# Kernel optimization log

Measured on AMD Instinct MI355X. Metric: run time of the kernel, lower is better.

The kernel has to match this reference:

```python
import jax, jax.numpy as jnp
import numpy as np

HIDDEN = 1024
CUTOFFS = [20000, 80000, 200000]
PROJECT_FACTOR = 4
NUM_TAILS = len(CUTOFFS) - 1
CUTOFF_ENDS = [0] + CUTOFFS
BATCH, SEQ = 8, 1024


def _glorot(key, shape):
    fan_in, fan_out = shape
    limit = np.sqrt(6.0 / (fan_in + fan_out)).astype(np.float32)
    return jax.random.uniform(key, shape, jnp.float32, -limit, limit)


def setup_inputs() -> dict:
    key = jax.random.key(0)
    ks = jax.random.split(key, 7)
    return {
        "x": jax.random.randint(ks[0], (BATCH, SEQ), 0, CUTOFFS[-1], dtype=jnp.int64.dtype if jax.config.jax_enable_x64 else jnp.int32),
        "head_weight_proj": _glorot(ks[1], (HIDDEN, HIDDEN)),
        "head_weight": _glorot(ks[2], (HIDDEN, CUTOFFS[0] + NUM_TAILS)),
        "tail_weight_proj_0": _glorot(ks[3], (HIDDEN, HIDDEN // PROJECT_FACTOR)),
        "tail_weight_0": _glorot(ks[4], (HIDDEN // PROJECT_FACTOR, CUTOFFS[1] - CUTOFFS[0])),
        "tail_weight_proj_1": _glorot(ks[5], (HIDDEN, HIDDEN // PROJECT_FACTOR ** 2)),
        "tail_weight_1": _glorot(ks[6], (HIDDEN // PROJECT_FACTOR ** 2, CUTOFFS[2] - CUTOFFS[1])),
    }


def reference(x, head_weight_proj, head_weight, tail_weight_proj_0,
              tail_weight_0, tail_weight_proj_1, tail_weight_1) -> jnp.ndarray:
    # Faithful to AdaptiveEmbedding.compute_embeddings:
    #   tables[i] = weight.T (head truncated to cutoffs[0] rows), projs[i] = proj.T
    #   per-cluster: gather rows of table for in-range ids, matmul with proj,
    #   scatter back into y; here expressed densely with masks (same math,
    #   fixed shapes; out-of-cluster tokens contribute exactly zero).
    tables = [head_weight.T[:CUTOFFS[0]], tail_weight_0.T, tail_weight_1.T]
    projs = [head_weight_proj.T, tail_weight_proj_0.T, tail_weight_proj_1.T]
    y = jnp.zeros(x.shape + (HIDDEN,), dtype=jnp.float32)
    for i in range(len(CUTOFF_ENDS) - 1):
        l_idx, r_idx = CUTOFF_ENDS[i], CUTOFF_ENDS[i + 1]
        mask = (x >= l_idx) & (x < r_idx)                  # [B,S]
        idx = jnp.where(mask, x - l_idx, 0)                # in-range gather ids
        emb = tables[i][idx]                               # [B,S,d_i]
        proj = jnp.einsum('bsd,dh->bsh', emb, projs[i])    # [B,S,H]
        y = y + jnp.where(mask[..., None], proj, 0.0)
    emb_scale = jnp.asarray(HIDDEN ** 0.5, y.dtype)
    return y * emb_scale
```

## Files before the change

kernel.cpp:

```cpp
#include <hip/hip_runtime.h>
#include <hip/hip_bf16.h>

#define NTOK 8192
#define HID 1024
#define C0_END 20000
#define C1_END 80000
#define S0 20002
#define S1 60000
#define S2 120000

#define CAP0 1280
#define CAP1 3072
#define CAP2 6144
#define TS0 (CAP0/32)
#define TS1 (CAP1/32)
#define TS2 (CAP2/32)

#define NBUCK 12500

#define OFF_CNT 0
#define OFF_SST 16
#define OFF_BB  32
#define OFF_LS  50048
#define OFF_LI  (OFF_LS + NTOK*3*4)
#define OFF_W0  (OFF_LI + NTOK*3*4)
#define OFF_W1  (OFF_W0 + 1024*1024*2)
#define OFF_W2  (OFF_W1 + 256*1024*2)
#define OFF_A0  (OFF_W2 + 64*1024*2)
#define OFF_A1  (OFF_A0 + CAP0*1024*2)
#define OFF_A2  (OFF_A1 + CAP1*256*2)

typedef __attribute__((ext_vector_type(8))) short bf16x8;
typedef __attribute__((ext_vector_type(8))) unsigned short ushort8;
typedef __attribute__((ext_vector_type(4))) float f32x4;

__device__ __forceinline__ unsigned short f2bf(float f) {
    union { __hip_bfloat16 b; unsigned short u; } cv;
    cv.b = __float2bfloat16(f);
    return cv.u;
}


__global__ void k_init(unsigned* __restrict__ bb, int* __restrict__ cnt) {
    int gid = blockIdx.x * 256 + threadIdx.x, stride = gridDim.x * 256;
    for (int i = gid; i < NBUCK; i += stride) bb[i] = 0u;
    if (gid < 3) cnt[gid] = 0;
}

__global__ void k_count(const int* __restrict__ x, int* __restrict__ cnt,
                        unsigned* __restrict__ bb) {
    int s = blockIdx.x * 256 + threadIdx.x;
    int lane = threadIdx.x & 63;
    int v = x[s];
    atomicAdd(&bb[v >> 4], 1u);
    int c = (v < C0_END) ? 0 : (v < C1_END ? 1 : 2);
    unsigned long long m0 = __ballot(c == 0);
    unsigned long long m1 = __ballot(c == 1);
    unsigned long long m2 = __ballot(c == 2);
    unsigned long long mymask = (c == 0) ? m0 : (c == 1) ? m1 : m2;
    int leader = __builtin_ctzll(mymask);
    if (lane == leader) atomicAdd(&cnt[c], __popcll(mymask));
}

__global__ __launch_bounds__(1024) void k_scan(unsigned* __restrict__ bb,
                                               unsigned* __restrict__ sstart) {
    __shared__ unsigned psum[16];
    int t = threadIdx.x, lane = t & 63, w = t >> 6;
    int base = t * 13;
    unsigned loc[13];
    unsigned s = 0;
#pragma unroll
    for (int i = 0; i < 13; i++) {
        int idx = base + i;
        unsigned v = (idx < NBUCK) ? bb[idx] : 0u;
        loc[i] = v; s += v;
    }
    unsigned inc = s;
    for (int d = 1; d < 64; d <<= 1) {
        unsigned o = __shfl_up(inc, d);
        if (lane >= d) inc += o;
    }
    if (lane == 63) psum[w] = inc;
    __syncthreads();
    if (w == 0) {
        unsigned ws = (lane < 16) ? psum[lane] : 0u;
        for (int d = 1; d < 16; d <<= 1) {
            unsigned o = __shfl_up(ws, d);
            if (lane >= d) ws += o;
        }
        if (lane < 16) psum[lane] = ws;
    }
    __syncthreads();
    unsigned excl = inc - s + ((w > 0) ? psum[w - 1] : 0u);
#pragma unroll
    for (int i = 0; i < 13; i++) {
        int idx = base + i;
        if (idx < NBUCK) bb[idx] = excl;
        excl += loc[i];
    }
    __syncthreads();
    if (t == 0) { sstart[0] = 0u; sstart[1] = bb[1250]; sstart[2] = bb[5000]; }
}

__global__ void k_scatter(const int* __restrict__ x, unsigned* __restrict__ bb,
                          const unsigned* __restrict__ sstart,
                          int* __restrict__ ls, int* __restrict__ li) {
    int s = blockIdx.x * 256 + threadIdx.x;
    int v = x[s];
    int c    = (v < C0_END) ? 0 : (v < C1_END ? 1 : 2);
    int base = (c == 0) ? 0 : (c == 1) ? C0_END : C1_END;
    unsigned cap = (c == 0) ? CAP0 : (c == 1) ? CAP1 : CAP2;
    unsigned pos = atomicAdd(&bb[v >> 4], 1u) - sstart[c];
    if (pos < cap) {
        ls[c * NTOK + pos] = s;
        li[c * NTOK + pos] = v - base;
    }
}

template <int KS>
__device__ __forceinline__ size_t frag_off(int m, int k8) {
    return ((size_t)(((m >> 5) * KS + (k8 >> 2)) * 2 + ((m >> 4) & 1)) << 9)
         + (size_t)(((m & 15) + (k8 & 3) * 16) * 8);
}

template <int KS, int S, int MGSH>
__device__ __forceinline__ void spread_item(int e, int mi, int ki, int n,
                                            const float* __restrict__ t,
                                            const int* __restrict__ li,
                                            unsigned short* __restrict__ A) {
    int mg  = e >> MGSH;
    int k8g = e & ((1 << MGSH) - 1);
    int m  = mg * 8 + mi;
    int k8 = k8g * 8 + ki;
    int idx = (m < n) ? li[m] : 0;
    const float* src = t + (size_t)(k8 * 8) * S + idx;
    ushort8 v = {0, 0, 0, 0, 0, 0, 0, 0};
    if (m < n) {
#pragma unroll
        for (int j = 0; j < 8; j++) v[j] = f2bf(src[(size_t)j * S]);
    }
    *(ushort8*)(A + frag_off<KS>(m, k8)) = v;
}

__global__ void k_gather(const float* __restrict__ t0, const float* __restrict__ t1,
                         const float* __restrict__ t2,
                         const float* __restrict__ hwp, const float* __restrict__ twp0,
                         const float* __restrict__ twp1,
                         const int* __restrict__ cnt, const int* __restrict__ li,
                         unsigned short* __restrict__ A0, unsigned short* __restrict__ A1,
                         unsigned short* __restrict__ A2,
                         unsigned short* __restrict__ W0, unsigned short* __restrict__ W1,
                         unsigned short* __restrict__ W2) {
    int gid = blockIdx.x * 256 + threadIdx.x, stride = gridDim.x * 256;
    for (int i = gid; i < (1024 * 1024) / 4; i += stride) {
        float4 v = ((const float4*)hwp)[i];
        ushort4 o = { f2bf(v.x), f2bf(v.y), f2bf(v.z), f2bf(v.w) };
        ((ushort4*)W0)[i] = o;
    }
    for (int i = gid; i < (1024 * 256) / 4; i += stride) {
        float4 v = ((const float4*)twp0)[i];
        ushort4 o = { f2bf(v.x), f2bf(v.y), f2bf(v.z), f2bf(v.w) };
        ((ushort4*)W1)[i] = o;
    }
    for (int i = gid; i < (1024 * 64) / 4; i += stride) {
        float4 v = ((const float4*)twp1)[i];
        ushort4 o = { f2bf(v.x), f2bf(v.y), f2bf(v.z), f2bf(v.w) };
        ((ushort4*)W2)[i] = o;
    }
    int n0 = min(cnt[0], CAP0), n1 = min(cnt[1], CAP1), n2 = min(cnt[2], CAP2);
    int r0 = ((n0 + 31) >> 5) << 5;
    int r1 = ((n1 + 31) >> 5) << 5;
    int r2 = ((n2 + 31) >> 5) << 5;
    int i0 = r0 * 2;
    int i1 = r1 / 2;
    int i2 = r2 / 8;
    int tot = i0 + i1 + i2;
    int lane = threadIdx.x & 63;
    int mi = lane >> 3, ki = lane & 7;
    int wid = blockIdx.x * (blockDim.x >> 6) + (threadIdx.x >> 6);
    int nw  = gridDim.x * (blockDim.x >> 6);
    for (int it = wid; it < tot; it += nw) {
        if (it < i0)
            spread_item<32, S0, 4>(it, mi, ki, n0, t0, li, A0);
        else if (it < i0 + i1)
            spread_item<8, S1, 2>(it - i0, mi, ki, n1, t1, li + NTOK, A1);
        else
            spread_item<2, S2, 0>(it - i0 - i1, mi, ki, n2, t2, li + 2 * NTOK, A2);
    }
}

template <int K>
__device__ __forceinline__ void gemm_body(int tile, int n, int lane, int wave, int by,
                                          const unsigned short* __restrict__ Ap,
                                          const unsigned short* __restrict__ Wb,
                                          const int* __restrict__ ls,
                                          float* __restrict__ out) {
    constexpr int KS = K / 32;
    int m0 = tile * 32;
    int lr = lane & 15, lg = lane >> 4;
    int hb = by * 256 + wave * 64;
    const unsigned short* abase = Ap + (size_t)tile * KS * 1024 + lane * 8;
    const unsigned short* bbase = Wb + (size_t)(hb + lr) * K + lg * 8;
    f32x4 acc[2][4] = {};
#pragma unroll 4
    for (int ks = 0; ks < KS; ks++) {
        bf16x8 a0 = *(const bf16x8*)(abase + ks * 1024);
        bf16x8 a1 = *(const bf16x8*)(abase + ks * 1024 + 512);
        bf16x8 b0 = *(const bf16x8*)(bbase + ks * 32);
        bf16x8 b1 = *(const bf16x8*)(bbase + ks * 32 + 16 * K);
        bf16x8 b2 = *(const bf16x8*)(bbase + ks * 32 + 32 * K);
        bf16x8 b3 = *(const bf16x8*)(bbase + ks * 32 + 48 * K);
        acc[0][0] = __builtin_amdgcn_mfma_f32_16x16x32_bf16(a0, b0, acc[0][0], 0, 0, 0);
        acc[0][1] = __builtin_amdgcn_mfma_f32_16x16x32_bf16(a0, b1, acc[0][1], 0, 0, 0);
        acc[0][2] = __builtin_amdgcn_mfma_f32_16x16x32_bf16(a0, b2, acc[0][2], 0, 0, 0);
        acc[0][3] = __builtin_amdgcn_mfma_f32_16x16x32_bf16(a0, b3, acc[0][3], 0, 0, 0);
        acc[1][0] = __builtin_amdgcn_mfma_f32_16x16x32_bf16(a1, b0, acc[1][0], 0, 0, 0);
        acc[1][1] = __builtin_amdgcn_mfma_f32_16x16x32_bf16(a1, b1, acc[1][1], 0, 0, 0);
        acc[1][2] = __builtin_amdgcn_mfma_f32_16x16x32_bf16(a1, b2, acc[1][2], 0, 0, 0);
        acc[1][3] = __builtin_amdgcn_mfma_f32_16x16x32_bf16(a1, b3, acc[1][3], 0, 0, 0);
    }
#pragma unroll
    for (int mf = 0; mf < 2; mf++)
#pragma unroll
        for (int r = 0; r < 4; r++) {
            int m = mf * 16 + lg * 4 + r;
            if (m0 + m < n) {
                int s = ls[m0 + m];
                float* orow = out + (size_t)s * HID + hb + lr;
                orow[0]  = 32.f * acc[mf][0][r];
                orow[16] = 32.f * acc[mf][1][r];
                orow[32] = 32.f * acc[mf][2][r];
                orow[48] = 32.f * acc[mf][3][r];
            }
        }
}

__global__ __launch_bounds__(256) void k_gemm(const int* __restrict__ cnt,
                                              const int* __restrict__ ls,
                                              const unsigned short* __restrict__ A0,
                                              const unsigned short* __restrict__ A1,
                                              const unsigned short* __restrict__ A2,
                                              const unsigned short* __restrict__ W0,
                                              const unsigned short* __restrict__ W1,
                                              const unsigned short* __restrict__ W2,
                                              float* __restrict__ out) {
    int bx = blockIdx.x;
    int lane = threadIdx.x & 63, wave = threadIdx.x >> 6;
    if (bx < TS0) {
        int n = min(cnt[0], CAP0); if (bx * 32 >= n) return;
        gemm_body<1024>(bx, n, lane, wave, blockIdx.y, A0, W0, ls, out);
    } else if (bx < TS0 + TS1) {
        int t = bx - TS0;
        int n = min(cnt[1], CAP1); if (t * 32 >= n) return;
        gemm_body<256>(t, n, lane, wave, blockIdx.y, A1, W1, ls + NTOK, out);
    } else {
        int t = bx - TS0 - TS1;
        int n = min(cnt[2], CAP2); if (t * 32 >= n) return;
        gemm_body<64>(t, n, lane, wave, blockIdx.y, A2, W2, ls + 2 * NTOK, out);
    }
}

extern "C" void kernel_launch(void* const* d_in, const int* in_sizes, int n_in,
                              void* d_out, int out_size, void* d_ws, size_t ws_size,
                              hipStream_t stream) {
    const int*   x    = (const int*)d_in[0];
    const float* hwp  = (const float*)d_in[1];
    const float* hw   = (const float*)d_in[2];
    const float* twp0 = (const float*)d_in[3];
    const float* tw0  = (const float*)d_in[4];
    const float* twp1 = (const float*)d_in[5];
    const float* tw1  = (const float*)d_in[6];

    char* ws = (char*)d_ws;
    int* cnt          = (int*)(ws + OFF_CNT);
    unsigned* sstart  = (unsigned*)(ws + OFF_SST);
    unsigned* bb      = (unsigned*)(ws + OFF_BB);
    int* ls           = (int*)(ws + OFF_LS);
    int* li           = (int*)(ws + OFF_LI);
    unsigned short* W0 = (unsigned short*)(ws + OFF_W0);
    unsigned short* W1 = (unsigned short*)(ws + OFF_W1);
    unsigned short* W2 = (unsigned short*)(ws + OFF_W2);
    unsigned short* A0 = (unsigned short*)(ws + OFF_A0);
    unsigned short* A1 = (unsigned short*)(ws + OFF_A1);
    unsigned short* A2 = (unsigned short*)(ws + OFF_A2);
    float* out = (float*)d_out;

    k_init<<<64, 256, 0, stream>>>(bb, cnt);
    k_count<<<NTOK / 256, 256, 0, stream>>>(x, cnt, bb);
    k_scan<<<1, 1024, 0, stream>>>(bb, sstart);
    k_scatter<<<NTOK / 256, 256, 0, stream>>>(x, bb, sstart, ls, li);
    k_gather<<<1024, 256, 0, stream>>>(hw, tw0, tw1, hwp, twp0, twp1,
                                       cnt, li, A0, A1, A2, W0, W1, W2);
    k_gemm<<<dim3(TS0 + TS1 + TS2, 4), 256, 0, stream>>>(
        cnt, ls, A0, A1, A2, W0, W1, W2, out);
}
```

Measured before the change: 78.50 us.

## Fuse bucket-sort preprocessing into one kernel using shared-memory histogram

Replaces the four preprocessing kernels (init, count, scan, scatter) with a single kernel. Block 0 does the histogram, scan and scatter entirely in shared memory, while the other 256 blocks convert the projection weights to bf16 concurrently, and that conversion is taken out of the gather kernel. The aim is to cut launch overhead and global atomics, and to overlap the weight conversion with the sort. The cost is that the whole sort now runs serially on one workgroup, and the 50KB shared histogram may limit occupancy.

```diff
diff --git a/kernel.cpp b/kernel.cpp
--- a/kernel.cpp
+++ b/kernel.cpp
@@ -20,8 +20,7 @@
 
 #define OFF_CNT 0
 #define OFF_SST 16
-#define OFF_BB  32
-#define OFF_LS  50048
+#define OFF_LS  64
 #define OFF_LI  (OFF_LS + NTOK*3*4)
 #define OFF_W0  (OFF_LI + NTOK*3*4)
 #define OFF_W1  (OFF_W0 + 1024*1024*2)
@@ -40,80 +39,92 @@
     return cv.u;
 }
 
-
-__global__ void k_init(unsigned* __restrict__ bb, int* __restrict__ cnt) {
-    int gid = blockIdx.x * 256 + threadIdx.x, stride = gridDim.x * 256;
-    for (int i = gid; i < NBUCK; i += stride) bb[i] = 0u;
-    if (gid < 3) cnt[gid] = 0;
-}
-
-__global__ void k_count(const int* __restrict__ x, int* __restrict__ cnt,
-                        unsigned* __restrict__ bb) {
-    int s = blockIdx.x * 256 + threadIdx.x;
-    int lane = threadIdx.x & 63;
-    int v = x[s];
-    atomicAdd(&bb[v >> 4], 1u);
-    int c = (v < C0_END) ? 0 : (v < C1_END ? 1 : 2);
-    unsigned long long m0 = __ballot(c == 0);
-    unsigned long long m1 = __ballot(c == 1);
-    unsigned long long m2 = __ballot(c == 2);
-    unsigned long long mymask = (c == 0) ? m0 : (c == 1) ? m1 : m2;
-    int leader = __builtin_ctzll(mymask);
-    if (lane == leader) atomicAdd(&cnt[c], __popcll(mymask));
-}
-
-__global__ __launch_bounds__(1024) void k_scan(unsigned* __restrict__ bb,
-                                               unsigned* __restrict__ sstart) {
+__global__ __launch_bounds__(1024) void k_pre(
+        const int* __restrict__ x, int* __restrict__ cnt,
+        unsigned* __restrict__ sstart, int* __restrict__ ls, int* __restrict__ li,
+        const float* __restrict__ hwp, const float* __restrict__ twp0,
+        const float* __restrict__ twp1,
+        unsigned short* __restrict__ W0, unsigned short* __restrict__ W1,
+        unsigned short* __restrict__ W2) {
+    __shared__ unsigned hist[NBUCK];
     __shared__ unsigned psum[16];
-    int t = threadIdx.x, lane = t & 63, w = t >> 6;
-    int base = t * 13;
-    unsigned loc[13];
-    unsigned s = 0;
-#pragma unroll
-    for (int i = 0; i < 13; i++) {
-        int idx = base + i;
-        unsigned v = (idx < NBUCK) ? bb[idx] : 0u;
-        loc[i] = v; s += v;
-    }
-    unsigned inc = s;
-    for (int d = 1; d < 64; d <<= 1) {
-        unsigned o = __shfl_up(inc, d);
-        if (lane >= d) inc += o;
-    }
-    if (lane == 63) psum[w] = inc;
-    __syncthreads();
-    if (w == 0) {
-        unsigned ws = (lane < 16) ? psum[lane] : 0u;
-        for (int d = 1; d < 16; d <<= 1) {
-            unsigned o = __shfl_up(ws, d);
-            if (lane >= d) ws += o;
-        }
-        if (lane < 16) psum[lane] = ws;
-    }
-    __syncthreads();
-    unsigned excl = inc - s + ((w > 0) ? psum[w - 1] : 0u);
-#pragma unroll
-    for (int i = 0; i < 13; i++) {
-        int idx = base + i;
-        if (idx < NBUCK) bb[idx] = excl;
-        excl += loc[i];
-    }
-    __syncthreads();
-    if (t == 0) { sstart[0] = 0u; sstart[1] = bb[1250]; sstart[2] = bb[5000]; }
-}
-
-__global__ void k_scatter(const int* __restrict__ x, unsigned* __restrict__ bb,
-                          const unsigned* __restrict__ sstart,
-                          int* __restrict__ ls, int* __restrict__ li) {
-    int s = blockIdx.x * 256 + threadIdx.x;
-    int v = x[s];
-    int c    = (v < C0_END) ? 0 : (v < C1_END ? 1 : 2);
-    int base = (c == 0) ? 0 : (c == 1) ? C0_END : C1_END;
-    unsigned cap = (c == 0) ? CAP0 : (c == 1) ? CAP1 : CAP2;
-    unsigned pos = atomicAdd(&bb[v >> 4], 1u) - sstart[c];
-    if (pos < cap) {
-        ls[c * NTOK + pos] = s;
-        li[c * NTOK + pos] = v - base;
+    __shared__ unsigned sstl[3];
+    if (blockIdx.x == 0) {
+        int t = threadIdx.x, lane = t & 63, w = t >> 6;
+        for (int i = t; i < NBUCK; i += 1024) hist[i] = 0u;
+        __syncthreads();
+        for (int i = t; i < NTOK; i += 1024)
+            atomicAdd(&hist[x[i] >> 4], 1u);
+        __syncthreads();
+        int base = t * 13;
+        unsigned loc[13];
+        unsigned s = 0;
+#pragma unroll
+        for (int i = 0; i < 13; i++) {
+            int idx = base + i;
+            unsigned v = (idx < NBUCK) ? hist[idx] : 0u;
+            loc[i] = v; s += v;
+        }
+        unsigned inc = s;
+        for (int d = 1; d < 64; d <<= 1) {
+            unsigned o = __shfl_up(inc, d);
+            if (lane >= d) inc += o;
+        }
+        if (lane == 63) psum[w] = inc;
+        __syncthreads();
+        if (w == 0) {
+            unsigned wsv = (lane < 16) ? psum[lane] : 0u;
+            for (int d = 1; d < 16; d <<= 1) {
+                unsigned o = __shfl_up(wsv, d);
+                if (lane >= d) wsv += o;
+            }
+            if (lane < 16) psum[lane] = wsv;
+        }
+        __syncthreads();
+        unsigned excl = inc - s + ((w > 0) ? psum[w - 1] : 0u);
+#pragma unroll
+        for (int i = 0; i < 13; i++) {
+            int idx = base + i;
+            if (idx < NBUCK) hist[idx] = excl;
+            excl += loc[i];
+        }
+        __syncthreads();
+        if (t == 0) {
+            unsigned s1 = hist[1250], s2 = hist[5000];
+            sstl[0] = 0u; sstl[1] = s1; sstl[2] = s2;
+            sstart[0] = 0u; sstart[1] = s1; sstart[2] = s2;
+            cnt[0] = (int)s1; cnt[1] = (int)(s2 - s1); cnt[2] = (int)(NTOK - s2);
+        }
+        __syncthreads();
+        for (int i = t; i < NTOK; i += 1024) {
+            int v = x[i];
+            int c    = (v < C0_END) ? 0 : (v < C1_END ? 1 : 2);
+            int bse  = (c == 0) ? 0 : (c == 1) ? C0_END : C1_END;
+            unsigned cap = (c == 0) ? CAP0 : (c == 1) ? CAP1 : CAP2;
+            unsigned pos = atomicAdd(&hist[v >> 4], 1u) - sstl[c];
+            if (pos < cap) {
+                ls[c * NTOK + pos] = i;
+                li[c * NTOK + pos] = v - bse;
+            }
+        }
+    } else {
+        int gid = (blockIdx.x - 1) * 1024 + threadIdx.x;
+        int stride = (gridDim.x - 1) * 1024;
+        for (int i = gid; i < (1024 * 1024) / 4; i += stride) {
+            float4 v = ((const float4*)hwp)[i];
+            ushort4 o = { f2bf(v.x), f2bf(v.y), f2bf(v.z), f2bf(v.w) };
+            ((ushort4*)W0)[i] = o;
+        }
+        for (int i = gid; i < (1024 * 256) / 4; i += stride) {
+            float4 v = ((const float4*)twp0)[i];
+            ushort4 o = { f2bf(v.x), f2bf(v.y), f2bf(v.z), f2bf(v.w) };
+            ((ushort4*)W1)[i] = o;
+        }
+        for (int i = gid; i < (1024 * 64) / 4; i += stride) {
+            float4 v = ((const float4*)twp1)[i];
+            ushort4 o = { f2bf(v.x), f2bf(v.y), f2bf(v.z), f2bf(v.w) };
+            ((ushort4*)W2)[i] = o;
+        }
     }
 }
 
@@ -144,29 +155,9 @@
 
 __global__ void k_gather(const float* __restrict__ t0, const float* __restrict__ t1,
                          const float* __restrict__ t2,
-                         const float* __restrict__ hwp, const float* __restrict__ twp0,
-                         const float* __restrict__ twp1,
                          const int* __restrict__ cnt, const int* __restrict__ li,
                          unsigned short* __restrict__ A0, unsigned short* __restrict__ A1,
-                         unsigned short* __restrict__ A2,
-                         unsigned short* __restrict__ W0, unsigned short* __restrict__ W1,
-                         unsigned short* __restrict__ W2) {
-    int gid = blockIdx.x * 256 + threadIdx.x, stride = gridDim.x * 256;
-    for (int i = gid; i < (1024 * 1024) / 4; i += stride) {
-        float4 v = ((const float4*)hwp)[i];
-        ushort4 o = { f2bf(v.x), f2bf(v.y), f2bf(v.z), f2bf(v.w) };
-        ((ushort4*)W0)[i] = o;
-    }
-    for (int i = gid; i < (1024 * 256) / 4; i += stride) {
-        float4 v = ((const float4*)twp0)[i];
-        ushort4 o = { f2bf(v.x), f2bf(v.y), f2bf(v.z), f2bf(v.w) };
-        ((ushort4*)W1)[i] = o;
-    }
-    for (int i = gid; i < (1024 * 64) / 4; i += stride) {
-        float4 v = ((const float4*)twp1)[i];
-        ushort4 o = { f2bf(v.x), f2bf(v.y), f2bf(v.z), f2bf(v.w) };
-        ((ushort4*)W2)[i] = o;
-    }
+                         unsigned short* __restrict__ A2) {
     int n0 = min(cnt[0], CAP0), n1 = min(cnt[1], CAP1), n2 = min(cnt[2], CAP2);
     int r0 = ((n0 + 31) >> 5) << 5;
     int r1 = ((n1 + 31) >> 5) << 5;
@@ -274,7 +265,6 @@
     char* ws = (char*)d_ws;
     int* cnt          = (int*)(ws + OFF_CNT);
     unsigned* sstart  = (unsigned*)(ws + OFF_SST);
-    unsigned* bb      = (unsigned*)(ws + OFF_BB);
     int* ls           = (int*)(ws + OFF_LS);
     int* li           = (int*)(ws + OFF_LI);
     unsigned short* W0 = (unsigned short*)(ws + OFF_W0);
@@ -285,12 +275,9 @@
     unsigned short* A2 = (unsigned short*)(ws + OFF_A2);
     float* out = (float*)d_out;
 
-    k_init<<<64, 256, 0, stream>>>(bb, cnt);
-    k_count<<<NTOK / 256, 256, 0, stream>>>(x, cnt, bb);
-    k_scan<<<1, 1024, 0, stream>>>(bb, sstart);
-    k_scatter<<<NTOK / 256, 256, 0, stream>>>(x, bb, sstart, ls, li);
-    k_gather<<<1024, 256, 0, stream>>>(hw, tw0, tw1, hwp, twp0, twp1,
-                                       cnt, li, A0, A1, A2, W0, W1, W2);
+    k_pre<<<257, 1024, 0, stream>>>(x, cnt, sstart, ls, li,
+                                    hwp, twp0, twp1, W0, W1, W2);
+    k_gather<<<1024, 256, 0, stream>>>(hw, tw0, tw1, cnt, li, A0, A1, A2);
     k_gemm<<<dim3(TS0 + TS1 + TS2, 4), 256, 0, stream>>>(
         cnt, ls, A0, A1, A2, W0, W1, W2, out);
 }
```

New measurement: 72.32 us, median of 2. -7.9%, faster.
